# Kernel tuning notes

Hardware: AMD Instinct MI355X
Metric: run time of the kernel (lower is better)

The kernel has to match this reference:

```python
import jax, jax.numpy as jnp
import numpy as np

B = 4096      # number of queries
N = 65536     # number of reference points

def setup_inputs() -> dict:
    key = jax.random.key(0)
    k1, k2, k3 = jax.random.split(key, 3)
    x = jax.random.normal(k1, (B,), dtype=jnp.float32)
    input_tensor = jax.random.normal(k2, (N,), dtype=jnp.float32)
    accuracy_tensor = jax.random.uniform(k3, (N,), dtype=jnp.float32)
    return {"x": x, "input_tensor": input_tensor, "accuracy_tensor": accuracy_tensor}

def reference(x, input_tensor, accuracy_tensor):
    # (B, N) broadcast abs-difference distance matrix
    distances = jnp.abs(input_tensor[None, :] - x[:, None])
    # nearest reference point per query
    min_idx = jnp.argmin(distances, axis=1)          # (B,)
    return accuracy_tensor[min_idx]                  # (B,)
```

## Files before the change

kernel.cpp:

```cpp
#include <hip/hip_runtime.h>

#define QB 4

__global__ __launch_bounds__(256, 4)
void nn_kernel(const float* __restrict__ x,
               const float* __restrict__ pts,
               const float* __restrict__ acc,
               float* __restrict__ out,
               int B, int N) {
    const int lane = threadIdx.x & 63;
    const int wave = threadIdx.x >> 6;
    const int q    = blockIdx.x * QB + wave;
    if (q >= B) return;

    const float xq = x[q];

    const int G = N >> 2;
    const int J = G >> 6;

    float bd0 = __builtin_inff(), bd1 = __builtin_inff(),
          bd2 = __builtin_inff(), bd3 = __builtin_inff();
    int   bj0 = 0, bj1 = 0, bj2 = 0, bj3 = 0;

    const float4* __restrict__ p4 = reinterpret_cast<const float4*>(pts);

    #pragma unroll 4
    for (int j = 0; j < J; ++j) {
        float4 v = p4[lane + 64 * j];
        float d0 = fabsf(v.x - xq);
        float d1 = fabsf(v.y - xq);
        float d2 = fabsf(v.z - xq);
        float d3 = fabsf(v.w - xq);
        if (d0 < bd0) { bd0 = d0; bj0 = j; }
        if (d1 < bd1) { bd1 = d1; bj1 = j; }
        if (d2 < bd2) { bd2 = d2; bj2 = j; }
        if (d3 < bd3) { bd3 = d3; bj3 = j; }
    }

    unsigned long long key;
    {
        unsigned i0 = (unsigned)(4 * (lane + 64 * bj0) + 0);
        unsigned i1 = (unsigned)(4 * (lane + 64 * bj1) + 1);
        unsigned i2 = (unsigned)(4 * (lane + 64 * bj2) + 2);
        unsigned i3 = (unsigned)(4 * (lane + 64 * bj3) + 3);
        unsigned long long k0 = ((unsigned long long)__float_as_uint(bd0) << 32) | i0;
        unsigned long long k1 = ((unsigned long long)__float_as_uint(bd1) << 32) | i1;
        unsigned long long k2 = ((unsigned long long)__float_as_uint(bd2) << 32) | i2;
        unsigned long long k3 = ((unsigned long long)__float_as_uint(bd3) << 32) | i3;
        key = k0 < k1 ? k0 : k1;
        unsigned long long k23 = k2 < k3 ? k2 : k3;
        key = key < k23 ? key : k23;
    }

    for (int i = J * 256 + lane; i < N; i += 64) {
        float d = fabsf(pts[i] - xq);
        unsigned long long k = ((unsigned long long)__float_as_uint(d) << 32) | (unsigned)i;
        key = key < k ? key : k;
    }

    #pragma unroll
    for (int off = 1; off < 64; off <<= 1) {
        unsigned long long o = __shfl_xor(key, off, 64);
        key = key < o ? key : o;
    }

    if (lane == 0) {
        out[q] = acc[(unsigned)(key & 0xffffffffULL)];
    }
}

extern "C" void kernel_launch(void* const* d_in, const int* in_sizes, int n_in,
                              void* d_out, int out_size, void* d_ws, size_t ws_size,
                              hipStream_t stream) {
    const float* x   = (const float*)d_in[0];
    const float* pts = (const float*)d_in[1];
    const float* acc = (const float*)d_in[2];
    float* out = (float*)d_out;
    const int B = in_sizes[0];
    const int N = in_sizes[1];
    const int blocks = (B + QB - 1) / QB;
    hipLaunchKernelGGL(nn_kernel, dim3(blocks), dim3(256), 0, stream,
                       x, pts, acc, out, B, N);
}
```

Measured before the change: 89.20 us.

## Split nearest-neighbor search into per-chunk partial argmin plus reduction kernel

Each lane now owns one query while the whole wave scans one 1024-point chunk, so the point loads are wave-uniform and can be served as scalar or broadcast reads. The per-query partial minima go to workspace and a second kernel reduces them. The old cross-lane shuffle reduction per query and the per-lane point loads are removed. In exchange it adds a second launch and workspace traffic of 64 chunks × B × 8 bytes, and it only runs when a large enough workspace is provided.

```diff
diff --git a/kernel.cpp b/kernel.cpp
--- a/kernel.cpp
+++ b/kernel.cpp
@@ -1,6 +1,82 @@
 #include <hip/hip_runtime.h>
 
+#define CHUNK 1024
 #define QB 4
+
+__global__ __launch_bounds__(256, 4)
+void nn_part_kernel(const float* __restrict__ x,
+                    const float* __restrict__ pts,
+                    unsigned long long* __restrict__ part,
+                    int B, int qw_shift)
+{
+    const int lane = threadIdx.x & 63;
+    const int wv = __builtin_amdgcn_readfirstlane((int)(threadIdx.x >> 6));
+    const int w  = blockIdx.x * 4 + wv;
+    const int qw = w & ((1 << qw_shift) - 1);
+    const int ck = w >> qw_shift;
+
+    const int q = (qw << 6) + lane;
+    const float xq = x[q];
+
+    const float* __restrict__ pc = pts + (size_t)ck * CHUNK;
+
+    const float inf = __builtin_inff();
+    float bd0 = inf, bd1 = inf, bd2 = inf, bd3 = inf;
+    int bj0 = 0, bj1 = 1, bj2 = 2, bj3 = 3;
+
+    #pragma unroll 8
+    for (int g = 0; g < CHUNK / 4; ++g) {
+        float p0 = pc[4 * g + 0];
+        float p1 = pc[4 * g + 1];
+        float p2 = pc[4 * g + 2];
+        float p3 = pc[4 * g + 3];
+        float d0 = fabsf(p0 - xq);
+        float d1 = fabsf(p1 - xq);
+        float d2 = fabsf(p2 - xq);
+        float d3 = fabsf(p3 - xq);
+        if (d0 < bd0) { bd0 = d0; bj0 = 4 * g + 0; }
+        if (d1 < bd1) { bd1 = d1; bj1 = 4 * g + 1; }
+        if (d2 < bd2) { bd2 = d2; bj2 = 4 * g + 2; }
+        if (d3 < bd3) { bd3 = d3; bj3 = 4 * g + 3; }
+    }
+
+    const unsigned base = (unsigned)ck * (unsigned)CHUNK;
+    unsigned long long k0 = ((unsigned long long)__float_as_uint(bd0) << 32) | (base + (unsigned)bj0);
+    unsigned long long k1 = ((unsigned long long)__float_as_uint(bd1) << 32) | (base + (unsigned)bj1);
+    unsigned long long k2 = ((unsigned long long)__float_as_uint(bd2) << 32) | (base + (unsigned)bj2);
+    unsigned long long k3 = ((unsigned long long)__float_as_uint(bd3) << 32) | (base + (unsigned)bj3);
+    unsigned long long ka = k0 < k1 ? k0 : k1;
+    unsigned long long kb = k2 < k3 ? k2 : k3;
+    unsigned long long key = ka < kb ? ka : kb;
+
+    part[(size_t)ck * B + q] = key;
+}
+
+__global__ __launch_bounds__(256, 4)
+void nn_reduce_kernel(const unsigned long long* __restrict__ part,
+                      const float* __restrict__ acc,
+                      float* __restrict__ out,
+                      int B, int nchunk)
+{
+    const int lane = threadIdx.x & 63;
+    const int wv   = threadIdx.x >> 6;
+    const int q    = blockIdx.x * 4 + wv;
+    if (q >= B) return;
+
+    unsigned long long key = ~0ULL;
+    for (int c = lane; c < nchunk; c += 64) {
+        unsigned long long k = part[(size_t)c * B + q];
+        key = k < key ? k : key;
+    }
+    #pragma unroll
+    for (int off = 1; off < 64; off <<= 1) {
+        unsigned long long o = __shfl_xor(key, off, 64);
+        key = key < o ? key : o;
+    }
+    if (lane == 0) {
+        out[q] = acc[(unsigned)(key & 0xffffffffULL)];
+    }
+}
 
 __global__ __launch_bounds__(256, 4)
 void nn_kernel(const float* __restrict__ x,
@@ -14,7 +90,6 @@
     if (q >= B) return;
 
     const float xq = x[q];
-
     const int G = N >> 2;
     const int J = G >> 6;
 
@@ -78,7 +153,27 @@
     float* out = (float*)d_out;
     const int B = in_sizes[0];
     const int N = in_sizes[1];
-    const int blocks = (B + QB - 1) / QB;
-    hipLaunchKernelGGL(nn_kernel, dim3(blocks), dim3(256), 0, stream,
-                       x, pts, acc, out, B, N);
+
+    const int nchunk = N / CHUNK;
+    const int nqw    = B >> 6;
+    const size_t need = (size_t)nchunk * (size_t)B * 8;
+
+    const bool pow2 = (nqw > 0) && ((nqw & (nqw - 1)) == 0);
+    const bool fast = (N % CHUNK == 0) && (B % 64 == 0) && pow2 &&
+                      d_ws != nullptr && ws_size >= need;
+
+    if (fast) {
+        int qw_shift = 0;
+        while ((1 << qw_shift) < nqw) ++qw_shift;
+        const int waves  = nchunk * nqw;
+        const int blocks = waves / 4;
+        hipLaunchKernelGGL(nn_part_kernel, dim3(blocks), dim3(256), 0, stream,
+                           x, pts, (unsigned long long*)d_ws, B, qw_shift);
+        hipLaunchKernelGGL(nn_reduce_kernel, dim3((B + 3) / 4), dim3(256), 0, stream,
+                           (const unsigned long long*)d_ws, acc, out, B, nchunk);
+    } else {
+        const int blocks = (B + QB - 1) / QB;
+        hipLaunchKernelGGL(nn_kernel, dim3(blocks), dim3(256), 0, stream,
+                           x, pts, acc, out, B, N);
+    }
 }
```

Measured after the change: 101.2 us. 13.5% more time.

## Split reference points into LDS chunks with one query per thread and atomicMin merge

Applied to the files above, without the earlier changes.

Restructures the search so each block stages a 512-point chunk in LDS and every thread handles one query, scanning the chunk with fminf in groups of 32 and tracking the group where the minimum was reached. The exact index is recovered by rescanning only that group, and partial results are merged across chunks with a 64-bit atomicMin on a packed (distance, index) key in workspace. Separate init and gather kernels are added. This swaps per-wave global loads and per-element compare/select bookkeeping for LDS broadcast reads and cheaper min ops, at the cost of three launches and many global atomics.

```diff
diff --git a/kernel.cpp b/kernel.cpp
--- a/kernel.cpp
+++ b/kernel.cpp
@@ -1,6 +1,84 @@
 #include <hip/hip_runtime.h>
 
-#define QB 4
+#define CHUNK 512
+#define GRP   32
+#define QB    4
+
+__global__ __launch_bounds__(256, 8)
+void nn_init_kernel(unsigned long long* __restrict__ best, int B) {
+    int i = blockIdx.x * 256 + threadIdx.x;
+    if (i < B) best[i] = ~0ULL;
+}
+
+__global__ __launch_bounds__(256, 8)
+void nn_main_kernel(const float* __restrict__ x,
+                    const float* __restrict__ pts,
+                    unsigned long long* __restrict__ best,
+                    int qg_shift)
+{
+    __shared__ float lds[CHUNK];
+    const int tid = threadIdx.x;
+    const int nqg_mask = (1 << qg_shift) - 1;
+    const int qg = blockIdx.x & nqg_mask;
+    const int ck = blockIdx.x >> qg_shift;
+
+    reinterpret_cast<float2*>(lds)[tid] =
+        reinterpret_cast<const float2*>(pts)[ck * (CHUNK / 2) + tid];
+    __syncthreads();
+
+    const int lane = tid & 63;
+    const int wv   = tid >> 6;
+    const int q    = (qg << 8) + (wv << 6) + lane;
+    const float xq = x[q];
+
+    const float inf = __builtin_inff();
+    float bdA = inf, bdB = inf, prev = inf;
+    int grp = 0;
+
+    const float4* __restrict__ l4 = reinterpret_cast<const float4*>(lds);
+
+    #pragma unroll 2
+    for (int g = 0; g < CHUNK / GRP; ++g) {
+        #pragma unroll
+        for (int t = 0; t < GRP / 4; ++t) {
+            float4 v = l4[g * (GRP / 4) + t];
+            float d0 = v.x - xq;
+            float d1 = v.y - xq;
+            float d2 = v.z - xq;
+            float d3 = v.w - xq;
+            bdA = fminf(fminf(fabsf(d0), fabsf(d1)), bdA);
+            bdB = fminf(fminf(fabsf(d2), fabsf(d3)), bdB);
+        }
+        float cur = fminf(bdA, bdB);
+        grp  = (cur < prev) ? g : grp;
+        prev = cur;
+    }
+
+    const float bd = prev;
+
+    int bi = 0;
+    #pragma unroll
+    for (int t = GRP / 4 - 1; t >= 0; --t) {
+        float4 v = l4[grp * (GRP / 4) + t];
+        bi = (fabsf(v.w - xq) == bd) ? 4 * t + 3 : bi;
+        bi = (fabsf(v.z - xq) == bd) ? 4 * t + 2 : bi;
+        bi = (fabsf(v.y - xq) == bd) ? 4 * t + 1 : bi;
+        bi = (fabsf(v.x - xq) == bd) ? 4 * t + 0 : bi;
+    }
+
+    const unsigned gidx = (unsigned)(ck * CHUNK + grp * GRP + bi);
+    const unsigned long long key =
+        ((unsigned long long)__float_as_uint(bd) << 32) | gidx;
+    atomicMin(&best[q], key);
+}
+
+__global__ __launch_bounds__(256, 8)
+void nn_gather_kernel(const unsigned long long* __restrict__ best,
+                      const float* __restrict__ acc,
+                      float* __restrict__ out, int B) {
+    int i = blockIdx.x * 256 + threadIdx.x;
+    if (i < B) out[i] = acc[(unsigned)(best[i] & 0xffffffffULL)];
+}
 
 __global__ __launch_bounds__(256, 4)
 void nn_kernel(const float* __restrict__ x,
@@ -14,7 +92,6 @@
     if (q >= B) return;
 
     const float xq = x[q];
-
     const int G = N >> 2;
     const int J = G >> 6;
 
@@ -78,7 +155,27 @@
     float* out = (float*)d_out;
     const int B = in_sizes[0];
     const int N = in_sizes[1];
-    const int blocks = (B + QB - 1) / QB;
-    hipLaunchKernelGGL(nn_kernel, dim3(blocks), dim3(256), 0, stream,
-                       x, pts, acc, out, B, N);
+
+    const int nqg = B >> 8;
+    const bool pow2 = (nqg > 0) && ((nqg & (nqg - 1)) == 0);
+    const bool fast = pow2 && (B % 256 == 0) && (N % CHUNK == 0) &&
+                      d_ws != nullptr && ws_size >= (size_t)B * 8;
+
+    if (fast) {
+        int qg_shift = 0;
+        while ((1 << qg_shift) < nqg) ++qg_shift;
+        const int nchunk = N / CHUNK;
+        unsigned long long* best = (unsigned long long*)d_ws;
+
+        hipLaunchKernelGGL(nn_init_kernel, dim3(nqg), dim3(256), 0, stream,
+                           best, B);
+        hipLaunchKernelGGL(nn_main_kernel, dim3(nchunk * nqg), dim3(256), 0,
+                           stream, x, pts, best, qg_shift);
+        hipLaunchKernelGGL(nn_gather_kernel, dim3(nqg), dim3(256), 0, stream,
+                           best, acc, out, B);
+    } else {
+        const int blocks = (B + QB - 1) / QB;
+        hipLaunchKernelGGL(nn_kernel, dim3(blocks), dim3(256), 0, stream,
+                           x, pts, acc, out, B, N);
+    }
 }
```

Measured after the change: 71.78 us. -19.5%, faster.
